# Performance work log

Measured on AMD Instinct MI355X. Metric: run time of the kernel, lower is better.

## Reference

```python
import jax, jax.numpy as jnp
import numpy as np

EMBED_DIM = 1024
NUM_HEADS = 16
HEAD_DIM = EMBED_DIM // NUM_HEADS


def setup_inputs() -> dict:
    key = jax.random.key(0)
    kx, kq, kk, kv, kbq, kbk, kbv = jax.random.split(key, 7)
    s = 1.0 / np.sqrt(EMBED_DIM)
    return {
        "x": jax.random.normal(kx, (4, 2048, EMBED_DIM), dtype=jnp.float32),
        "Wq": jax.random.uniform(kq, (EMBED_DIM, EMBED_DIM), jnp.float32, -s, s),
        "bq": jax.random.uniform(kbq, (EMBED_DIM,), jnp.float32, -s, s),
        "Wk": jax.random.uniform(kk, (EMBED_DIM, EMBED_DIM), jnp.float32, -s, s),
        "bk": jax.random.uniform(kbk, (EMBED_DIM,), jnp.float32, -s, s),
        "Wv": jax.random.uniform(kv, (EMBED_DIM, EMBED_DIM), jnp.float32, -s, s),
        "bv": jax.random.uniform(kbv, (EMBED_DIM,), jnp.float32, -s, s),
    }


def reference(x, Wq, bq, Wk, bk, Wv, bv):
    B, S, E = x.shape
    H, D = NUM_HEADS, HEAD_DIM
    # QKV projections; reshape to (B, H, S, D)
    def proj(W, b):
        return (x @ W + b).reshape(B, S, H, D).transpose(0, 2, 1, 3)
    Q = proj(Wq, bq)
    K = proj(Wk, bk)
    V = proj(Wv, bv)
    scale = jnp.asarray(np.sqrt(D), x.dtype)
    scores = jnp.einsum("bhqd,bhkd->bhqk", Q, K) / scale
    attn = jax.nn.softmax(scores, axis=-1)
    out = jnp.einsum("bhqk,bhkd->bhqd", attn, V)
    return out.transpose(0, 2, 1, 3).reshape(B, S, E)
```

## Files before the change

### kernel.cpp

```cpp
#include <hip/hip_runtime.h>
#include <math.h>

typedef unsigned short u16;
typedef __bf16 bf16x8 __attribute__((ext_vector_type(8)));
typedef float f32x4 __attribute__((ext_vector_type(4)));
typedef u16 u16x8 __attribute__((ext_vector_type(8)));
typedef u16 u16x4 __attribute__((ext_vector_type(4)));
typedef short s16x4 __attribute__((ext_vector_type(4)));
typedef unsigned u32x2 __attribute__((ext_vector_type(2)));
typedef unsigned u32x4 __attribute__((ext_vector_type(4)));

#define BB 4
#define SS 2048
#define EE 1024
#define HH 16
#define DH 64
#define PLANE (SS * DH)

__device__ __forceinline__ u16 f32_to_bf16(float f) {
  unsigned u = __builtin_bit_cast(unsigned, f);
  u += 0x7fffu + ((u >> 16) & 1u);
  return (u16)(u >> 16);
}

__device__ __forceinline__ unsigned pack_bf16_trunc(float lo, float hi) {
  return __builtin_amdgcn_perm(__builtin_bit_cast(unsigned, hi),
                               __builtin_bit_cast(unsigned, lo), 0x07060302u);
}

__device__ __forceinline__ void async_copy16(const void* g, void* lds) {
  __builtin_amdgcn_global_load_lds(
      (const __attribute__((address_space(1))) void*)g,
      (__attribute__((address_space(3))) void*)lds, 16, 0, 0);
}

__device__ __forceinline__ float ex2(float x) {
#if __has_builtin(__builtin_amdgcn_exp2f)
  return __builtin_amdgcn_exp2f(x);
#else
  float r;
  asm("v_exp_f32 %0, %1\n\ts_nop 1" : "=v"(r) : "v"(x));
  return r;
#endif
}

__global__ __launch_bounds__(256) void cvt_kernel(
    const float* __restrict__ x, const float* __restrict__ Wq,
    const float* __restrict__ Wk, const float* __restrict__ Wv,
    u16* __restrict__ xb, u16* __restrict__ wb) {
  __shared__ u16 T[64 * 72];
  int bid = blockIdx.x;
  int t = threadIdx.x;
  if (bid < 4096) {
    int i = (bid * 256 + t) * 8;
    float4 a = *(const float4*)(x + i);
    float4 c = *(const float4*)(x + i + 4);
    u16x8 o;
    o[0] = f32_to_bf16(a.x); o[1] = f32_to_bf16(a.y);
    o[2] = f32_to_bf16(a.z); o[3] = f32_to_bf16(a.w);
    o[4] = f32_to_bf16(c.x); o[5] = f32_to_bf16(c.y);
    o[6] = f32_to_bf16(c.z); o[7] = f32_to_bf16(c.w);
    *(u16x8*)(xb + i) = o;
    return;
  }
  int wid = bid - 4096;
  int mat = wid >> 8, r = wid & 255;
  const float* W = (mat == 0) ? Wq : ((mat == 1) ? Wk : Wv);
  int e0 = (r & 15) * 64, k0 = (r >> 4) * 64;
  int tr = t >> 4, tc = t & 15;
  for (int i = 0; i < 4; ++i) {
    int k = i * 16 + tr;
    float4 v = *(const float4*)(W + (k0 + k) * EE + e0 + tc * 4);
    T[(tc * 4 + 0) * 72 + k] = f32_to_bf16(v.x);
    T[(tc * 4 + 1) * 72 + k] = f32_to_bf16(v.y);
    T[(tc * 4 + 2) * 72 + k] = f32_to_bf16(v.z);
    T[(tc * 4 + 3) * 72 + k] = f32_to_bf16(v.w);
  }
  __syncthreads();
  u16* out = wb + (size_t)(mat * EE + e0) * EE + k0;
  for (int i = 0; i < 4; ++i) {
    int e = i * 16 + tr;
    u16x4 v = *(u16x4*)&T[e * 72 + tc * 4];
    *(u16x4*)(out + e * EE + tc * 4) = v;
  }
}

__global__ __launch_bounds__(256) void qkv_gemm_kernel(
    const u16* __restrict__ A, const u16* __restrict__ Bt,
    const float* __restrict__ bq, const float* __restrict__ bk,
    const float* __restrict__ bv, u16* __restrict__ qkv) {
  __shared__ u16 As0[128 * 64], Bs0[128 * 64];
  __shared__ u16 As1[128 * 64], Bs1[128 * 64];
  int tid = threadIdx.x;
  int lane = tid & 63, w = tid >> 6;
  int ln = lane & 15, quad = lane >> 4;
  int wm = w & 1, wn = w >> 1;
  int bn = blockIdx.x, bm = blockIdx.y;
  const u16* Ag = A + (size_t)bm * 128 * EE;
  const u16* Bg = Bt + (size_t)bn * 128 * EE;

  int r8 = lane >> 3, c8 = lane & 7;
  int sc8 = (c8 ^ r8) * 8;

  f32x4 acc[4][4] = {};

  auto STAGE = [&](u16* AsD, u16* BsD, int kt) {
    int k0 = kt * 64;
#pragma unroll
    for (int i = 0; i < 4; ++i) {
      int row0 = i * 32 + w * 8;
      async_copy16(Ag + (row0 + r8) * EE + k0 + sc8, AsD + (i * 256 + w * 64) * 8);
      async_copy16(Bg + (row0 + r8) * EE + k0 + sc8, BsD + (i * 256 + w * 64) * 8);
    }
  };

  int k7 = ln & 7;
  int ks0 = (quad ^ k7) * 8;
  int ks1 = ks0 ^ 32;

  auto TILE = [&](const u16* AsB, const u16* BsB) {
    __builtin_amdgcn_s_setprio(1);
    bf16x8 b0[4], b1[4];
#pragma unroll
    for (int ni = 0; ni < 4; ++ni) {
      const u16* br = BsB + (wn * 64 + ni * 16 + ln) * 64;
      b0[ni] = *(const bf16x8*)(br + ks0);
      b1[ni] = *(const bf16x8*)(br + ks1);
    }
#pragma unroll
    for (int mi = 0; mi < 4; ++mi) {
      const u16* ar = AsB + (wm * 64 + mi * 16 + ln) * 64;
      bf16x8 a0 = *(const bf16x8*)(ar + ks0);
      bf16x8 a1 = *(const bf16x8*)(ar + ks1);
#pragma unroll
      for (int ni = 0; ni < 4; ++ni) {
        acc[mi][ni] = __builtin_amdgcn_mfma_f32_16x16x32_bf16(a0, b0[ni],
                                                              acc[mi][ni], 0, 0, 0);
        acc[mi][ni] = __builtin_amdgcn_mfma_f32_16x16x32_bf16(a1, b1[ni],
                                                              acc[mi][ni], 0, 0, 0);
      }
    }
    __builtin_amdgcn_s_setprio(0);
  };

  STAGE(As0, Bs0, 0);
#pragma unroll 1
  for (int kt = 0; kt < 16; kt += 2) {
    STAGE(As1, Bs1, kt + 1);
    asm volatile("s_waitcnt vmcnt(8)" ::: "memory");
    __builtin_amdgcn_sched_barrier(0);
    __builtin_amdgcn_s_barrier();
    __builtin_amdgcn_sched_barrier(0);
    TILE(As0, Bs0);
    __builtin_amdgcn_s_barrier();
    if (kt + 2 < 16) {
      STAGE(As0, Bs0, kt + 2);
      asm volatile("s_waitcnt vmcnt(8)" ::: "memory");
    } else {
      asm volatile("s_waitcnt vmcnt(0)" ::: "memory");
    }
    __builtin_amdgcn_sched_barrier(0);
    __builtin_amdgcn_s_barrier();
    __builtin_amdgcn_sched_barrier(0);
    TILE(As1, Bs1);
    __builtin_amdgcn_s_barrier();
  }

  int mat = bn >> 3;
  const float* bias = (mat == 0) ? bq : ((mat == 1) ? bk : bv);
  int b = bm >> 4;
  if (mat < 2) {
    float scl = (mat == 0) ? 0.18033688011112042f : 1.0f;
    int base0 = (mat * BB + b) * HH * PLANE;
    for (int ni = 0; ni < 4; ++ni) {
      int e = (bn & 7) * 128 + wn * 64 + ni * 16 + ln;
      float bve = bias[e];
      int hh = e >> 6, d = e & 63;
      int cb = base0 + hh * PLANE + d;
      for (int mi = 0; mi < 4; ++mi) {
        int s0 = (bm & 15) * 128 + wm * 64 + mi * 16 + quad * 4;
        for (int r = 0; r < 4; ++r)
          qkv[cb + (s0 + r) * DH] = f32_to_bf16((acc[mi][ni][r] + bve) * scl);
      }
    }
  } else {
    size_t base0 = (size_t)(2 * BB + b) * HH * PLANE;
    for (int ni = 0; ni < 4; ++ni) {
      int e = (bn & 7) * 128 + wn * 64 + ni * 16 + ln;
      float bve = bias[e];
      int hh = e >> 6, d = e & 63;
      size_t cb = base0 + (size_t)hh * PLANE + (size_t)d * SS;
      for (int mi = 0; mi < 4; ++mi) {
        int s0 = (bm & 15) * 128 + wm * 64 + mi * 16 + quad * 4;
        u16x4 vv;
        for (int r = 0; r < 4; ++r) vv[r] = f32_to_bf16(acc[mi][ni][r] + bve);
        *(u16x4*)(qkv + cb + s0) = vv;
      }
    }
  }
}

__global__ __launch_bounds__(512, 4) void attn_kernel(const u16* __restrict__ qkv,
                                                      float* __restrict__ out) {
  __shared__ u16 Ks0[64 * 64], Ks1[64 * 64];
  __shared__ u16 Vs0[64 * 64], Vs1[64 * 64];
  int wg = blockIdx.x;
  int xcd = wg & 7, idx = wg >> 3;
  int bh = xcd * 8 + (idx >> 3);
  int qb = idx & 7;
  int h = bh & 15, b = bh >> 4;
  int t = threadIdx.x;
  int lane = t & 63, w = t >> 6;
  int ln = lane & 15, quad = lane >> 4;
  int k7 = ln & 7;
  int q0 = quad & 1, q1 = quad >> 1;
  const u16* Qg = qkv + (size_t)bh * PLANE + qb * 256 * DH;
  const u16* Kg = qkv + (size_t)(BB * HH + bh) * PLANE;
  const u16* Vg = qkv + (size_t)(2 * BB * HH + bh) * PLANE;

  int r8 = lane >> 3, c8 = lane & 7;
  int sc8 = (c8 ^ r8) * 8;

  auto STAGE = [&](u16* KsD, u16* VsD, int kt) {
    const u16* Kt = Kg + kt * 64 * DH;
    const u16* Vt = Vg + kt * 64;
    int row = w * 8 + r8;
    async_copy16(Kt + row * DH + sc8, KsD + (w * 8) * DH);
    async_copy16(Vt + row * SS + sc8, VsD + (w * 8) * DH);
  };

  bf16x8 bq[2][2];
#pragma unroll
  for (int rb = 0; rb < 2; ++rb)
#pragma unroll
    for (int s = 0; s < 2; ++s)
      bq[rb][s] = *(const bf16x8*)(Qg + (w * 32 + rb * 16 + ln) * DH + s * 32 + quad * 8);

  u32x4 ow;
  ow[0] = ow[1] = ow[2] = ow[3] = 0x3F803F80u;
  bf16x8 ones8 = __builtin_bit_cast(bf16x8, ow);

  const f32x4 kz = {};
  f32x4 o[4][2] = {};
  f32x4 lacc[2] = {};

  int ks0 = (quad ^ k7) * 8;
  int ks1 = ks0 ^ 32;

  auto TILE = [&](const u16* Ksb, const u16* Vsb) {
    __builtin_amdgcn_s_setprio(1);
    f32x4 s[2][4];
#pragma unroll
    for (int g = 0; g < 4; ++g) {
      const u16* krow = Ksb + (g * 16 + ln) * DH;
      bf16x8 kf0 = *(const bf16x8*)(krow + ks0);
      bf16x8 kf1 = *(const bf16x8*)(krow + ks1);
      s[0][g] = __builtin_amdgcn_mfma_f32_16x16x32_bf16(kf0, bq[0][0], kz, 0, 0, 0);
      s[0][g] = __builtin_amdgcn_mfma_f32_16x16x32_bf16(kf1, bq[0][1], s[0][g], 0, 0, 0);
      s[1][g] = __builtin_amdgcn_mfma_f32_16x16x32_bf16(kf0, bq[1][0], kz, 0, 0, 0);
      s[1][g] = __builtin_amdgcn_mfma_f32_16x16x32_bf16(kf1, bq[1][1], s[1][g], 0, 0, 0);
    }
    bf16x8 af[2][2];
#pragma unroll
    for (int rb = 0; rb < 2; ++rb) {
      unsigned Wd[4][2];
#pragma unroll
      for (int g = 0; g < 4; ++g) {
        Wd[g][0] = pack_bf16_trunc(ex2(s[rb][g][0]), ex2(s[rb][g][1]));
        Wd[g][1] = pack_bf16_trunc(ex2(s[rb][g][2]), ex2(s[rb][g][3]));
      }
#pragma unroll
      for (int G = 0; G < 2; ++G) {
        u32x4 aw;
        aw[0] = Wd[2 * G][0];     aw[1] = Wd[2 * G][1];
        aw[2] = Wd[2 * G + 1][0]; aw[3] = Wd[2 * G + 1][1];
        af[rb][G] = __builtin_bit_cast(bf16x8, aw);
      }
      lacc[rb] = __builtin_amdgcn_mfma_f32_16x16x32_bf16(af[rb][0], ones8, lacc[rb], 0, 0, 0);
      lacc[rb] = __builtin_amdgcn_mfma_f32_16x16x32_bf16(af[rb][1], ones8, lacc[rb], 0, 0, 0);
    }
#pragma unroll
    for (int G = 0; G < 2; ++G) {
      int uLo = ((4 * G + q1) ^ k7) * 8 + 4 * q0;
      int uHi = ((4 * G + q1 + 2) ^ k7) * 8 + 4 * q0;
#pragma unroll
      for (int dg = 0; dg < 4; ++dg) {
        const u16* vrow = Vsb + (dg * 16 + ln) * DH;
        u32x2 lo = *(const u32x2*)(vrow + uLo);
        u32x2 hi = *(const u32x2*)(vrow + uHi);
        u32x4 vv;
        vv[0] = lo[0]; vv[1] = lo[1]; vv[2] = hi[0]; vv[3] = hi[1];
        bf16x8 vf = __builtin_bit_cast(bf16x8, vv);
        o[dg][0] = __builtin_amdgcn_mfma_f32_16x16x32_bf16(af[0][G], vf, o[dg][0], 0, 0, 0);
        o[dg][1] = __builtin_amdgcn_mfma_f32_16x16x32_bf16(af[1][G], vf, o[dg][1], 0, 0, 0);
      }
    }
    __builtin_amdgcn_s_setprio(0);
  };

  STAGE(Ks0, Vs0, 0);
#pragma unroll 1
  for (int kt = 0; kt < 32; kt += 2) {
    STAGE(Ks1, Vs1, kt + 1);
    asm volatile("s_waitcnt vmcnt(2)" ::: "memory");
    __builtin_amdgcn_sched_barrier(0);
    __builtin_amdgcn_s_barrier();
    __builtin_amdgcn_sched_barrier(0);
    TILE(Ks0, Vs0);
    __builtin_amdgcn_s_barrier();
    if (kt + 2 < 32) {
      STAGE(Ks0, Vs0, kt + 2);
      asm volatile("s_waitcnt vmcnt(2)" ::: "memory");
    } else {
      asm volatile("s_waitcnt vmcnt(0)" ::: "memory");
    }
    __builtin_amdgcn_sched_barrier(0);
    __builtin_amdgcn_s_barrier();
    __builtin_amdgcn_sched_barrier(0);
    TILE(Ks1, Vs1);
    __builtin_amdgcn_s_barrier();
  }

  int sb = qb * 256 + w * 32;
  float* og = out + (size_t)b * SS * EE + (size_t)h * DH;
#pragma unroll
  for (int rb = 0; rb < 2; ++rb)
#pragma unroll
    for (int r = 0; r < 4; ++r) {
      float ir = 1.0f / lacc[rb][r];
      size_t qrow = (size_t)(sb + rb * 16 + quad * 4 + r);
#pragma unroll
      for (int dg = 0; dg < 4; ++dg)
        og[qrow * EE + dg * 16 + ln] = o[dg][rb][r] * ir;
    }
}

extern "C" void kernel_launch(void* const* d_in, const int* in_sizes, int n_in,
                              void* d_out, int out_size, void* d_ws, size_t ws_size,
                              hipStream_t stream) {
  (void)in_sizes; (void)n_in; (void)out_size; (void)ws_size;
  const float* x  = (const float*)d_in[0];
  const float* Wq = (const float*)d_in[1];
  const float* bq = (const float*)d_in[2];
  const float* Wk = (const float*)d_in[3];
  const float* bk = (const float*)d_in[4];
  const float* Wv = (const float*)d_in[5];
  const float* bv = (const float*)d_in[6];
  float* out = (float*)d_out;

  u16* xb  = (u16*)d_out;
  u16* wb  = xb + (size_t)BB * SS * EE;
  u16* qkv = (u16*)d_ws;

  cvt_kernel<<<dim3(4096 + 768), 256, 0, stream>>>(x, Wq, Wk, Wv, xb, wb);
  qkv_gemm_kernel<<<dim3(24, 64), 256, 0, stream>>>(xb, wb, bq, bk, bv, qkv);
  attn_kernel<<<dim3(512), 512, 0, stream>>>(qkv, out);
}
```

Before: 226.8 us.

## Stage two K/V tiles per barrier and permute V layout for 16-byte LDS reads

The attention loop now loads two 64-key K/V tiles per pipeline stage into doubled LDS buffers, which halves the number of barrier-separated stages and deepens the prefetch. The projection kernel writes V^T with a permuted column order within each 64-key tile, so the attention kernel can read each V fragment with one 16-byte LDS load instead of two 8-byte loads. This doubles LDS use per workgroup to 64 KB, which may lower occupancy against the 4-blocks launch bound.

```diff
diff --git a/kernel.cpp b/kernel.cpp
--- a/kernel.cpp
+++ b/kernel.cpp
@@ -191,10 +191,11 @@
       int hh = e >> 6, d = e & 63;
       size_t cb = base0 + (size_t)hh * PLANE + (size_t)d * SS;
       for (int mi = 0; mi < 4; ++mi) {
-        int s0 = (bm & 15) * 128 + wm * 64 + mi * 16 + quad * 4;
+        int tile = (bm & 15) * 2 + wm;
+        int L0 = quad * 16 + (mi >> 1) * 8 + (mi & 1) * 4;
         u16x4 vv;
         for (int r = 0; r < 4; ++r) vv[r] = f32_to_bf16(acc[mi][ni][r] + bve);
-        *(u16x4*)(qkv + cb + s0) = vv;
+        *(u16x4*)(qkv + cb + tile * 64 + L0) = vv;
       }
     }
   }
@@ -202,8 +203,8 @@
 
 __global__ __launch_bounds__(512, 4) void attn_kernel(const u16* __restrict__ qkv,
                                                       float* __restrict__ out) {
-  __shared__ u16 Ks0[64 * 64], Ks1[64 * 64];
-  __shared__ u16 Vs0[64 * 64], Vs1[64 * 64];
+  __shared__ u16 KA0[64 * 64], KA1[64 * 64], VA0[64 * 64], VA1[64 * 64];
+  __shared__ u16 KB0[64 * 64], KB1[64 * 64], VB0[64 * 64], VB1[64 * 64];
   int wg = blockIdx.x;
   int xcd = wg & 7, idx = wg >> 3;
   int bh = xcd * 8 + (idx >> 3);
@@ -213,7 +214,6 @@
   int lane = t & 63, w = t >> 6;
   int ln = lane & 15, quad = lane >> 4;
   int k7 = ln & 7;
-  int q0 = quad & 1, q1 = quad >> 1;
   const u16* Qg = qkv + (size_t)bh * PLANE + qb * 256 * DH;
   const u16* Kg = qkv + (size_t)(BB * HH + bh) * PLANE;
   const u16* Vg = qkv + (size_t)(2 * BB * HH + bh) * PLANE;
@@ -221,12 +221,14 @@
   int r8 = lane >> 3, c8 = lane & 7;
   int sc8 = (c8 ^ r8) * 8;
 
-  auto STAGE = [&](u16* KsD, u16* VsD, int kt) {
+  auto STAGE2 = [&](u16* K0, u16* V0, u16* K1, u16* V1, int kt) {
     const u16* Kt = Kg + kt * 64 * DH;
     const u16* Vt = Vg + kt * 64;
     int row = w * 8 + r8;
-    async_copy16(Kt + row * DH + sc8, KsD + (w * 8) * DH);
-    async_copy16(Vt + row * SS + sc8, VsD + (w * 8) * DH);
+    async_copy16(Kt + row * DH + sc8, K0 + (w * 8) * DH);
+    async_copy16(Vt + row * SS + sc8, V0 + (w * 8) * DH);
+    async_copy16(Kt + (64 + row) * DH + sc8, K1 + (w * 8) * DH);
+    async_copy16(Vt + row * SS + 64 + sc8, V1 + (w * 8) * DH);
   };
 
   bf16x8 bq[2][2];
@@ -281,16 +283,10 @@
     }
 #pragma unroll
     for (int G = 0; G < 2; ++G) {
-      int uLo = ((4 * G + q1) ^ k7) * 8 + 4 * q0;
-      int uHi = ((4 * G + q1 + 2) ^ k7) * 8 + 4 * q0;
 #pragma unroll
       for (int dg = 0; dg < 4; ++dg) {
         const u16* vrow = Vsb + (dg * 16 + ln) * DH;
-        u32x2 lo = *(const u32x2*)(vrow + uLo);
-        u32x2 hi = *(const u32x2*)(vrow + uHi);
-        u32x4 vv;
-        vv[0] = lo[0]; vv[1] = lo[1]; vv[2] = hi[0]; vv[3] = hi[1];
-        bf16x8 vf = __builtin_bit_cast(bf16x8, vv);
+        bf16x8 vf = *(const bf16x8*)(vrow + ((2 * quad + G) ^ k7) * 8);
         o[dg][0] = __builtin_amdgcn_mfma_f32_16x16x32_bf16(af[0][G], vf, o[dg][0], 0, 0, 0);
         o[dg][1] = __builtin_amdgcn_mfma_f32_16x16x32_bf16(af[1][G], vf, o[dg][1], 0, 0, 0);
       }
@@ -298,26 +294,28 @@
     __builtin_amdgcn_s_setprio(0);
   };
 
-  STAGE(Ks0, Vs0, 0);
+  STAGE2(KA0, VA0, KA1, VA1, 0);
 #pragma unroll 1
-  for (int kt = 0; kt < 32; kt += 2) {
-    STAGE(Ks1, Vs1, kt + 1);
-    asm volatile("s_waitcnt vmcnt(2)" ::: "memory");
-    __builtin_amdgcn_sched_barrier(0);
-    __builtin_amdgcn_s_barrier();
-    __builtin_amdgcn_sched_barrier(0);
-    TILE(Ks0, Vs0);
-    __builtin_amdgcn_s_barrier();
-    if (kt + 2 < 32) {
-      STAGE(Ks0, Vs0, kt + 2);
-      asm volatile("s_waitcnt vmcnt(2)" ::: "memory");
+  for (int rt = 0; rt < 32; rt += 4) {
+    STAGE2(KB0, VB0, KB1, VB1, rt + 2);
+    asm volatile("s_waitcnt vmcnt(4)" ::: "memory");
+    __builtin_amdgcn_sched_barrier(0);
+    __builtin_amdgcn_s_barrier();
+    __builtin_amdgcn_sched_barrier(0);
+    TILE(KA0, VA0);
+    TILE(KA1, VA1);
+    __builtin_amdgcn_s_barrier();
+    if (rt + 4 < 32) {
+      STAGE2(KA0, VA0, KA1, VA1, rt + 4);
+      asm volatile("s_waitcnt vmcnt(4)" ::: "memory");
     } else {
       asm volatile("s_waitcnt vmcnt(0)" ::: "memory");
     }
     __builtin_amdgcn_sched_barrier(0);
     __builtin_amdgcn_s_barrier();
     __builtin_amdgcn_sched_barrier(0);
-    TILE(Ks1, Vs1);
+    TILE(KB0, VB0);
+    TILE(KB1, VB1);
     __builtin_amdgcn_s_barrier();
   }
 
```

Measured after the change: 213.9 us. -5.7%, faster.
